# Kernel tuning notes

Measured on AMD Instinct MI355X. Metric: run time of the kernel, lower is better.

Reference implementation:

```python
import jax, jax.numpy as jnp
import numpy as np
from jax import lax

N_VERTICES = 2048  # matches init kwarg n_vertices and N


def setup_inputs() -> dict:
    key = jax.random.key(0)
    k1, k2, k3 = jax.random.split(key, 3)
    B, N, D, C = 16, N_VERTICES, 128, 8
    vertices = jax.random.normal(k1, (B, N, D), dtype=jnp.float32)
    # strictly-positive confidences -> max over classes is > 0 and distinct w.h.p.,
    # so each greedy step selects exactly one unvisited node (static output shape)
    confidence = jax.random.uniform(k2, (B, N, C), dtype=jnp.float32)
    neighbors = jax.random.randint(k3, (B, N, N), 0, 2).astype(jnp.float32)
    neighbors = neighbors * (1.0 - jnp.eye(N, dtype=jnp.float32))  # no self-loops
    return {"vertices": vertices, "confidence": confidence, "neighbors": neighbors}


def _propagate(vertices, confidence, neighbors):
    # vertices: [N, D]; confidence: [N, C]; neighbors: [N, N] binary
    N = vertices.shape[0]
    conf0 = jnp.max(confidence, axis=-1)  # [N]
    neg_inf = jnp.float32(-jnp.inf)

    def step(carry, _):
        conf, nbhd, unvis = carry  # [N] f32, [N] bool, [N] bool
        has_nbhd = jnp.any(nbhd)
        # pick max-confidence node from neighborhood, else global argmax
        fc_n = jnp.argmax(jnp.where(nbhd, conf, neg_inf))
        fc_a = jnp.argmax(conf)
        fc = jnp.where(has_nbhd, fc_n, fc_a)
        nbhd = nbhd.at[fc].set(False)  # neighborhood.remove(fc) (no-op if argmax branch)
        # add fc's still-unvisited neighbors (fc itself excluded: zero diagonal)
        nbhd = nbhd | ((neighbors[fc] == 1.0) & unvis)
        # zero out entries equal to conf[fc] (faithful to original tie-zeroing)
        conf = conf * (conf != conf[fc]).astype(conf.dtype)
        unvis = unvis.at[fc].set(False)
        return (conf, nbhd, unvis), fc

    init = (conf0, jnp.zeros(N, dtype=bool), jnp.ones(N, dtype=bool))
    _, perm = lax.scan(step, init, None, length=N)  # perm: [N] int
    return vertices[perm], perm.astype(jnp.int32)


def reference(vertices, confidence, neighbors):
    # returns (reordered vertices [B,N,D], reverse_map [B,N] int32)
    return jax.vmap(_propagate)(vertices, confidence, neighbors)
```

## Files before the change

kernel.cpp:

```cpp
#include <hip/hip_runtime.h>
#include <stdint.h>

#define BB 16
#define NN 2048
#define DD 128
#define CC 8

typedef unsigned long long u64;

__global__ __launch_bounds__(256, 1) void k_fused(const float* __restrict__ confid,
                                                  const float* __restrict__ nb,
                                                  float* __restrict__ perm_out) {
    __shared__ u64 keys[NN];
    __shared__ uint32_t hist[NN];
    __shared__ uint32_t sOrig[NN];
    __shared__ uint32_t sInv[NN];
    __shared__ float4 sRowV[NN / 4];
    __shared__ uint32_t sSing[64];
    __shared__ uint32_t sRs[64];
    __shared__ uint32_t wtot[8];

    int b = blockIdx.x, tid = threadIdx.x;
    int lane = tid & 63, wid = tid >> 6;
    const float* cb = confid + (size_t)b * NN * CC;

    u64 key[8]; int bkt[8];
#pragma unroll
    for (int q = 0; q < 8; q++) {
        int i = tid + q * 256;
        const float4* p4 = (const float4*)(cb + (size_t)i * CC);
        float4 a = p4[0], c = p4[1];
        float cf = fmaxf(fmaxf(fmaxf(a.x, a.y), fmaxf(a.z, a.w)),
                         fmaxf(fmaxf(c.x, c.y), fmaxf(c.z, c.w)));
        key[q] = ((u64)__float_as_uint(cf) << 32) | (uint32_t)(NN - 1 - i);
        float c2 = cf * cf, c4 = c2 * c2, c8 = c4 * c4;
        int ba = (int)(c8 * 2048.0f);
        ba = ba < 0 ? 0 : (ba > 2047 ? 2047 : ba);
        bkt[q] = 2047 - ba;
    }
#pragma unroll
    for (int q = 0; q < 8; q++) hist[tid + q * 256] = 0u;
    __syncthreads();
#pragma unroll
    for (int q = 0; q < 8; q++) atomicAdd(&hist[bkt[q]], 1u);
    __syncthreads();

    uint32_t v[8], run = 0;
#pragma unroll
    for (int q = 0; q < 8; q++) { v[q] = run; run += hist[tid * 8 + q]; }
    uint32_t inc = run;
#pragma unroll
    for (int s = 1; s < 64; s <<= 1) {
        uint32_t o = (uint32_t)__shfl_up((int)inc, s, 64);
        if (lane >= s) inc += o;
    }
    uint32_t wexc = inc - run;
    if (lane == 63) wtot[wid] = inc;
    __syncthreads();
    uint32_t wbase = 0;
    for (int ww = 0; ww < 4; ww++) if (ww < wid) wbase += wtot[ww];
    uint32_t tbase = wbase + wexc;
#pragma unroll
    for (int q = 0; q < 8; q++) hist[tid * 8 + q] = tbase + v[q];
    __syncthreads();

#pragma unroll
    for (int q = 0; q < 8; q++) {
        uint32_t pos = atomicAdd(&hist[bkt[q]], 1u);
        keys[pos] = key[q];
    }
    __syncthreads();

    {
        uint32_t segStart = (tid == 0) ? 0u : hist[tid * 8 - 1];
        for (int bq = 0; bq < 8; bq++) {
            uint32_t e = hist[tid * 8 + bq];
            for (uint32_t i = segStart + 1; i < e; i++) {
                u64 kk = keys[i];
                uint32_t j = i;
                while (j > segStart && keys[j - 1] < kk) { keys[j] = keys[j - 1]; j--; }
                keys[j] = kk;
            }
            segStart = e;
        }
    }
    __syncthreads();

    for (int p = tid; p < NN; p += 256) {
        uint32_t og = (uint32_t)(NN - 1) - (uint32_t)(keys[p] & 0xFFFFFFFFu);
        sOrig[p] = og;
        sInv[og] = (uint32_t)p;
    }
    __syncthreads();
    if (tid < 64) {
        uint32_t sw = 0, rw = 0;
        for (int k = 0; k < 32; k++) {
            int p = tid * 32 + k;
            uint32_t hc = (uint32_t)(keys[p] >> 32);
            bool isStart = (p == 0) || ((uint32_t)(keys[p - 1] >> 32) != hc);
            bool isEnd = (p == NN - 1) || ((uint32_t)(keys[p + 1] >> 32) != hc);
            rw |= isStart ? (1u << k) : 0u;
            sw |= (isStart && isEnd) ? (1u << k) : 0u;
        }
        sSing[tid] = sw;
        sRs[tid] = rw;
    }
    __syncthreads();

    const float* nbB = nb + (size_t)b * NN * NN;

    if (tid >= 64) {
        int w = tid - 64;
        int r = w >> 2, quarter = w & 3;
        const float* rowp = nbB + (size_t)sOrig[r] * NN + quarter * 512;
        float acc = 0;
#pragma unroll
        for (int j = 0; j < 32; j++) acc += rowp[j * 16];
        asm volatile("" :: "v"(acc));
        return;
    }

    float* po = perm_out + b * NN;
    float* sRowF = (float*)sRowV;

    uint32_t ocol[32];
#pragma unroll
    for (int k = 0; k < 32; k++) ocol[k] = sOrig[lane * 32 + k];

    uint32_t availW = 0xFFFFFFFFu, nbhdW = 0u, unvisW = 0xFFFFFFFFu;
    uint32_t nonSingW = ~sSing[lane];

    int t = 0;
    for (; t < NN; t++) {
        uint32_t w = nbhdW & availW;
        u64 m = __ballot(w != 0u);
        int p;
        bool positive;
        if (m) {
            int L = __ffsll(m) - 1;
            uint32_t wl = (uint32_t)__builtin_amdgcn_readlane((int)w, L);
            p = L * 32 + (__ffs(wl) - 1);
            positive = true;
        } else if (__ballot(nbhdW != 0u)) {
            uint32_t mo = 0xFFFFFFFFu;
#pragma unroll
            for (int k = 0; k < 32; k++)
                if (nbhdW & (1u << k)) mo = min(mo, ocol[k]);
#pragma unroll
            for (int s = 32; s; s >>= 1)
                mo = min(mo, (uint32_t)__shfl_xor((int)mo, s, 64));
            p = (int)sInv[mo];
            positive = false;
        } else {
            u64 ma = __ballot(availW != 0u);
            if (ma) {
                int L = __ffsll(ma) - 1;
                uint32_t wl = (uint32_t)__builtin_amdgcn_readlane((int)availW, L);
                p = L * 32 + (__ffs(wl) - 1);
                positive = true;
            } else {
                p = (int)sInv[0];
                positive = false;
            }
        }
        p = __builtin_amdgcn_readfirstlane(p);

        uint32_t ogv = sOrig[p];
        const float4* rv = (const float4*)(nbB + (size_t)ogv * NN);
#pragma unroll
        for (int c = 0; c < 8; c++)
            sRowV[c * 64 + lane] = rv[c * 64 + lane];
        uint32_t row = 0u;
#pragma unroll
        for (int k = 0; k < 32; k++)
            row |= (sRowF[ocol[k]] == 1.0f ? 1u : 0u) << k;

        if (lane == 0) po[t] = (float)ogv;

        uint32_t pbit = (lane == (p >> 5)) ? (1u << (p & 31)) : 0u;
        if (positive) {
            availW &= ~pbit;
            uint32_t nsw = (uint32_t)__builtin_amdgcn_readlane((int)nonSingW, p >> 5);
            if ((nsw >> (p & 31)) & 1u) {
                uint32_t hc = (uint32_t)(keys[p] >> 32);
                int rs = p, re = p;
                while (rs > 0 && (uint32_t)(keys[rs - 1] >> 32) == hc) rs--;
                while (re < NN - 1 && (uint32_t)(keys[re + 1] >> 32) == hc) re++;
                int lo = rs - lane * 32;     lo = lo < 0 ? 0 : (lo > 32 ? 32 : lo);
                int hi = re + 1 - lane * 32; hi = hi < 0 ? 0 : (hi > 32 ? 32 : hi);
                if (hi > lo) {
                    uint32_t mh = (hi >= 32) ? 0xFFFFFFFFu : ((1u << hi) - 1u);
                    uint32_t ml = (1u << lo) - 1u;
                    availW &= ~(mh & ~ml);
                }
            }
        }
        nbhdW  = (nbhdW & ~pbit) | (row & unvisW);
        unvisW &= ~pbit;

        uint32_t nnb = unvisW & ~nbhdW;
        if (__ballot(nnb != 0u) == 0ULL) { t++; break; }
    }

    if (t < NN) {
        uint32_t liveW = availW & unvisW;
        uint32_t rsW = sRs[lane];
        uint32_t pm = liveW & rsW;
        int cnt = __popc(pm);
        int inc2 = cnt;
#pragma unroll
        for (int s = 1; s < 64; s <<= 1) {
            int o = __shfl_up(inc2, s, 64);
            if (lane >= s) inc2 += o;
        }
        int pre = inc2 - cnt;
        int T2 = __shfl(inc2, 63, 64);

        int tt = t + pre;
#pragma unroll
        for (int k = 0; k < 32; k++) {
            if (pm & (1u << k)) { po[tt] = (float)ocol[k]; tt++; }
        }
        t += T2;

        uint32_t lm = unvisW & ~pm;
        while (__ballot(lm != 0u)) {
            uint32_t mo = 0xFFFFFFFFu;
#pragma unroll
            for (int k = 0; k < 32; k++)
                if (lm & (1u << k)) mo = min(mo, ocol[k]);
#pragma unroll
            for (int s = 32; s; s >>= 1)
                mo = min(mo, (uint32_t)__shfl_xor((int)mo, s, 64));
            if (lane == 0) po[t] = (float)mo;
            t++;
#pragma unroll
            for (int k = 0; k < 32; k++)
                if ((lm & (1u << k)) && ocol[k] == mo) lm &= ~(1u << k);
        }
    }
}

__global__ __launch_bounds__(256) void k_gather(const float* __restrict__ vtx,
                                                const float* __restrict__ perm_f,
                                                float* __restrict__ out0) {
    int tid = blockIdx.x * 256 + threadIdx.x;
    int d4 = tid & (DD / 4 - 1);
    int t  = (tid >> 5) & (NN - 1);
    int b  = tid >> 16;
    int p = (int)perm_f[b * NN + t];
    const float4* v4 = (const float4*)vtx;
    ((float4*)out0)[tid] = v4[(((size_t)b * NN + p) << 5) + d4];
}

extern "C" void kernel_launch(void* const* d_in, const int* in_sizes, int n_in,
                              void* d_out, int out_size, void* d_ws, size_t ws_size,
                              hipStream_t stream) {
    const float* vertices   = (const float*)d_in[0];
    const float* confidence = (const float*)d_in[1];
    const float* neighbors  = (const float*)d_in[2];

    float* out0     = (float*)d_out;
    float* perm_out = out0 + (size_t)BB * NN * DD;

    k_fused<<<BB, 256, 0, stream>>>(confidence, neighbors, perm_out);
    k_gather<<<(BB * NN * DD / 4) / 256, 256, 0, stream>>>(vertices, perm_out, out0);
}
```

Measured before the change: 40.00 us.

## Fuse gather into greedy kernel with per-batch flags for overlap

Merges the vertex gather into the greedy ordering kernel. Extra gather blocks spin on per-batch completion flags set with release stores, so each batch's rows are copied as soon as its permutation is ready instead of waiting for all batches and a second launch. This adds a flag-zeroing kernel and relies on all blocks being co-resident, since the spin-waiting blocks could otherwise deadlock. A two-kernel fallback is kept for when no workspace is available.

```diff
diff --git a/kernel.cpp b/kernel.cpp
--- a/kernel.cpp
+++ b/kernel.cpp
@@ -6,11 +6,22 @@
 #define DD 128
 #define CC 8
 
+#define NGREEDY 16
+#define NGATHER 752
+#define RPB 44
+
 typedef unsigned long long u64;
 
-__global__ __launch_bounds__(256, 1) void k_fused(const float* __restrict__ confid,
-                                                  const float* __restrict__ nb,
-                                                  float* __restrict__ perm_out) {
+__global__ void k_zero(uint32_t* __restrict__ flg) {
+    if (threadIdx.x < BB) flg[threadIdx.x] = 0u;
+}
+
+__global__ __launch_bounds__(256, 1) void k_main(const float* __restrict__ confid,
+                                                 const float* __restrict__ nb,
+                                                 const float* __restrict__ vtx,
+                                                 float* __restrict__ out0,
+                                                 float* __restrict__ perm_out,
+                                                 uint32_t* __restrict__ flg) {
     __shared__ u64 keys[NN];
     __shared__ uint32_t hist[NN];
     __shared__ uint32_t sOrig[NN];
@@ -20,7 +31,37 @@
     __shared__ uint32_t sRs[64];
     __shared__ uint32_t wtot[8];
 
-    int b = blockIdx.x, tid = threadIdx.x;
+    int tid = threadIdx.x;
+
+    if (blockIdx.x >= NGREEDY) {
+        int g = blockIdx.x - NGREEDY;
+        int row0 = g * RPB;
+        if (row0 >= BB * NN) return;
+        int rowL = min(row0 + RPB - 1, BB * NN - 1);
+        int bF = row0 >> 11, bL = rowL >> 11;
+        if (tid == 0) {
+            while (__hip_atomic_load(&flg[bF], __ATOMIC_ACQUIRE,
+                                     __HIP_MEMORY_SCOPE_AGENT) == 0u)
+                __builtin_amdgcn_s_sleep(8);
+            while (__hip_atomic_load(&flg[bL], __ATOMIC_ACQUIRE,
+                                     __HIP_MEMORY_SCOPE_AGENT) == 0u)
+                __builtin_amdgcn_s_sleep(8);
+        }
+        __syncthreads();
+        const float4* v4 = (const float4*)vtx;
+        float4* o4 = (float4*)out0;
+        for (int u = tid; u < RPB * (DD / 4); u += 256) {
+            int r = row0 + (u >> 5);
+            if (r >= BB * NN) break;
+            int d4 = u & 31;
+            int b = r >> 11;
+            int p = (int)perm_out[r];
+            o4[(size_t)r * 32 + d4] = v4[(((size_t)(b << 11) + p) << 5) + d4];
+        }
+        return;
+    }
+
+    int b = blockIdx.x;
     int lane = tid & 63, wid = tid >> 6;
     const float* cb = confid + (size_t)b * NN * CC;
 
@@ -239,11 +280,15 @@
                 if ((lm & (1u << k)) && ocol[k] == mo) lm &= ~(1u << k);
         }
     }
+
+    __threadfence();
+    if (lane == 0)
+        __hip_atomic_store(&flg[b], 1u, __ATOMIC_RELEASE, __HIP_MEMORY_SCOPE_AGENT);
 }
 
-__global__ __launch_bounds__(256) void k_gather(const float* __restrict__ vtx,
-                                                const float* __restrict__ perm_f,
-                                                float* __restrict__ out0) {
+__global__ __launch_bounds__(256) void k_gather_fb(const float* __restrict__ vtx,
+                                                   const float* __restrict__ perm_f,
+                                                   float* __restrict__ out0) {
     int tid = blockIdx.x * 256 + threadIdx.x;
     int d4 = tid & (DD / 4 - 1);
     int t  = (tid >> 5) & (NN - 1);
@@ -263,6 +308,15 @@
     float* out0     = (float*)d_out;
     float* perm_out = out0 + (size_t)BB * NN * DD;
 
-    k_fused<<<BB, 256, 0, stream>>>(confidence, neighbors, perm_out);
-    k_gather<<<(BB * NN * DD / 4) / 256, 256, 0, stream>>>(vertices, perm_out, out0);
+    if (ws_size >= 64) {
+        uint32_t* flg = (uint32_t*)d_ws;
+        k_zero<<<1, 64, 0, stream>>>(flg);
+        k_main<<<NGREEDY + NGATHER, 256, 0, stream>>>(confidence, neighbors,
+                                                      vertices, out0, perm_out, flg);
+    } else {
+        k_main<<<NGREEDY, 256, 0, stream>>>(confidence, neighbors,
+                                            vertices, out0, perm_out,
+                                            (uint32_t*)d_out );
+        k_gather_fb<<<(BB * NN * DD / 4) / 256, 256, 0, stream>>>(vertices, perm_out, out0);
+    }
 }
```

New measurement: 158.1 us. 3.95x slower.
